# Performance work log

Hardware: AMD Instinct MI355X
Metric: run time of the kernel (lower is better)

## Reference

```python
import jax, jax.numpy as jnp
import numpy as np


def setup_inputs() -> dict:
    key = jax.random.key(0)
    k1, k2, k3, k4, k5 = jax.random.split(key, 5)
    B, N, M, D = 4096, 2048, 2048, 9
    return {
        "x": jax.random.normal(k1, (B, N), dtype=jnp.float32),
        "eternal_weights": jax.random.normal(k2, (D, N, M), dtype=jnp.float32),
        "eternal_biases": jax.random.normal(k3, (M,), dtype=jnp.float32),
        "classical_weights": jax.random.normal(k4, (N, M), dtype=jnp.float32),
        "classical_biases": jax.random.normal(k5, (M,), dtype=jnp.float32),
    }


def _eternal_probs(eternal_weights, n, m):
    # The gate matrix is cos*I - sin*P + sin*P^T with P the circular shift,
    # so (gate @ s)[i] = cos*s[i] - sin*s[(i+1)%n] + sin*s[(i-1)%n].
    # Vectorize over all m output units at once: state is [m, n].
    state0 = jnp.full((m, n), 1.0 / np.sqrt(n), dtype=eternal_weights.dtype)
    angles = eternal_weights[:, :m, :3]  # [D, m, 3] -- weights[depth, j, 0/1/2]

    def gate(state, angle):  # angle: [m]
        c = jnp.cos(angle)[:, None]
        s = jnp.sin(angle)[:, None]
        return c * state - s * jnp.roll(state, -1, axis=1) + s * jnp.roll(state, 1, axis=1)

    def step(state, ang):  # ang: [m, 3] -- consciousness, intelligence, wisdom
        state = gate(state, ang[:, 0])
        state = gate(state, ang[:, 1])
        state = gate(state, ang[:, 2])
        return state, None

    state, _ = jax.lax.scan(step, state0, angles)
    return jnp.abs(state[:, 0]) ** 2  # [m]


def reference(x, eternal_weights, eternal_biases, classical_weights, classical_biases):
    # eternal_biases exists as a parameter in the original module but is unused in forward.
    n = x.shape[1]
    m = classical_weights.shape[1]
    classical = x @ classical_weights + classical_biases  # [B, m]
    probs = _eternal_probs(eternal_weights, n, m)  # [m], identical for every batch row
    return jnp.tanh(classical + probs[None, :])
```

## Files before the change

kernel.cpp:

```cpp
#include <hip/hip_runtime.h>
#include <hip/hip_fp8.h>
#include <stdint.h>

static constexpr int MM = 4096;
static constexpr int KK = 2048;
static constexpr int NN = 2048;

typedef float floatx16 __attribute__((ext_vector_type(16)));
typedef _Float16 f16x8 __attribute__((ext_vector_type(8)));
typedef unsigned short u16x8 __attribute__((ext_vector_type(8)));
typedef int intx4 __attribute__((ext_vector_type(4)));
typedef int intx8 __attribute__((ext_vector_type(8)));

__device__ __forceinline__ unsigned char f32_to_e4m3(float x) {
  __hip_fp8_e4m3 q(x);
  return (unsigned char)q.__x;
}
__device__ __forceinline__ float fast_tanh(float x) {
  float e = __expf(2.0f * x);
  return 1.0f - 2.0f / (e + 1.0f);
}
__device__ __forceinline__ unsigned short f32_to_f16_bits(float x) {
  union { _Float16 h; unsigned short u; } c; c.h = (_Float16)x;
  return c.u;
}
__device__ __forceinline__ float f16_bits_to_f32(unsigned short u) {
  union { _Float16 h; unsigned short u; } c; c.u = u;
  return (float)c.h;
}


__global__ __launch_bounds__(256) void prepass_kernel(
    const float* __restrict__ x, const float* __restrict__ E,
    const float* __restrict__ W, const float* __restrict__ cb,
    unsigned short* __restrict__ ahi, unsigned char* __restrict__ al8,
    unsigned short* __restrict__ bhi, unsigned char* __restrict__ bl8,
    float* __restrict__ bias2) {
  __shared__ float tile[64][65];
  const int blk = blockIdx.x;
  const int tid = threadIdx.x;

  if (blk < 2048) {
    int idx = blk * 256 + tid;
    int row = idx >> 7;
    int u = idx & 127;
    int g = u >> 2;
    int q = u & 3;
    const float4* s = (const float4*)(x + (size_t)row * KK + u * 16);
    float v[16];
#pragma unroll
    for (int p = 0; p < 4; p++) {
      float4 t = s[p];
      v[p * 4 + 0] = t.x; v[p * 4 + 1] = t.y; v[p * 4 + 2] = t.z; v[p * 4 + 3] = t.w;
    }
    unsigned short h[16];
    union { unsigned char b[16]; unsigned long long d[2]; } loq;
#pragma unroll
    for (int e = 0; e < 16; e++) {
      h[e] = f32_to_f16_bits(v[e]);
      float lo = v[e] - f16_bits_to_f32(h[e]);
      loq.b[e] = f32_to_e4m3(lo * 2048.0f);
    }
    size_t rb = (size_t)row * KK;
#pragma unroll
    for (int cc = 0; cc < 2; cc++) {
      int c8 = q * 2 + cc;
      int phys8 = (c8 + row + (row >> 3)) & 7;
      u16x8 o;
#pragma unroll
      for (int e = 0; e < 8; e++) o[e] = h[cc * 8 + e];
      *(u16x8*)(ahi + rb + g * 64 + phys8 * 8) = o;
    }
    {
      int sw = (row & 3) + ((row >> 2) & 3);
      int cA = (q >> 1) * 2;
      char* lb = (char*)al8 + rb + g * 64;
      *(unsigned long long*)(lb + (((cA + 0) + sw) & 3) * 16 + (q & 1) * 8) = loq.d[0];
      *(unsigned long long*)(lb + (((cA + 1) + sw) & 3) * 16 + (q & 1) * 8) = loq.d[1];
    }
  } else if (blk < 3072) {
    const int wb = blk - 2048;
    const int n0 = (wb & 31) * 64;
    const int k0 = (wb >> 5) * 64;
#pragma unroll
    for (int i = 0; i < 4; i++) {
      int t = tid + i * 256;
      int kr = t >> 4;
      int nc = (t & 15) * 4;
      const float4 vv = *(const float4*)(W + (size_t)(k0 + kr) * NN + n0 + nc);
      tile[nc + 0][kr] = vv.x;
      tile[nc + 1][kr] = vv.y;
      tile[nc + 2][kr] = vv.z;
      tile[nc + 3][kr] = vv.w;
    }
    __syncthreads();
    const int nl = tid >> 2;
    const int q = tid & 3;
    const int n = n0 + nl;
    float v[16];
    unsigned short h[16];
    union { unsigned char b[16]; unsigned long long d[2]; } loq;
#pragma unroll
    for (int e = 0; e < 16; e++) {
      v[e] = tile[nl][q * 16 + e];
      h[e] = f32_to_f16_bits(v[e]);
      float lo = v[e] - f16_bits_to_f32(h[e]);
      loq.b[e] = f32_to_e4m3(lo * 2048.0f);
    }
    size_t rb = (size_t)n * KK + k0;
#pragma unroll
    for (int cc = 0; cc < 2; cc++) {
      int c8 = q * 2 + cc;
      int phys8 = (c8 + n + (n >> 3)) & 7;
      u16x8 o;
#pragma unroll
      for (int e = 0; e < 8; e++) o[e] = h[cc * 8 + e];
      *(u16x8*)(bhi + rb + phys8 * 8) = o;
    }
    {
      int sw = (n & 3) + ((n >> 2) & 3);
      int cA = (q >> 1) * 2;
      char* lb = (char*)bl8 + rb;
      *(unsigned long long*)(lb + (((cA + 0) + sw) & 3) * 16 + (q & 1) * 8) = loq.d[0];
      *(unsigned long long*)(lb + (((cA + 1) + sw) & 3) * 16 + (q & 1) * 8) = loq.d[1];
    }
  } else {
    int i = (blk - 3072) * 256 + tid;
    if (i < NN) {
      float p = 1.0f / 2048.0f;
#pragma unroll
      for (int d = 0; d < 9; d++) {
        const float4 a = *(const float4*)(E + (size_t)d * (2048 * 2048) + (size_t)i * 2048);
        float c0 = cosf(a.x), c1 = cosf(a.y), c2 = cosf(a.z);
        p *= (c0 * c0) * (c1 * c1) * (c2 * c2);
      }
      bias2[i] = cb[i] + p;
    }
  }
}

#define GLL(dst, src)                                                        \
  __builtin_amdgcn_global_load_lds(                                          \
      (const __attribute__((address_space(1))) void*)(src),                  \
      (__attribute__((address_space(3))) void*)(dst), 16, 0, 0)

#define RD(S, CUR)                                                             \
  _Pragma("unroll") for (int t = 0; t < 2; t++) {                              \
    fa[S][t] = *(const f16x8*)(sAhB + (CUR) * 16384 + aho[S][t]);              \
    fb[S][t] = *(const f16x8*)(sBhB + (CUR) * 32768 + bho[S][t]);              \
  }

#define PERM(S)                                                                \
  _Pragma("unroll") for (int t = 0; t < 2; t++) {                              \
    const uint4 ua = *(const uint4*)&fa[S][t];                                 \
    fa8[t][2 * (S)]     = (int)__builtin_amdgcn_perm(ua.y, ua.x, 0x07050301u); \
    fa8[t][2 * (S) + 1] = (int)__builtin_amdgcn_perm(ua.w, ua.z, 0x07050301u); \
    const uint4 ub = *(const uint4*)&fb[S][t];                                 \
    fb8[t][2 * (S)]     = (int)__builtin_amdgcn_perm(ub.y, ub.x, 0x07050301u); \
    fb8[t][2 * (S) + 1] = (int)__builtin_amdgcn_perm(ub.w, ub.z, 0x07050301u); \
  }

#define MFMA4(S)                                                               \
  __builtin_amdgcn_s_setprio(1);                                               \
  _Pragma("unroll") for (int i = 0; i < 2; i++)                                \
    _Pragma("unroll") for (int j = 0; j < 2; j++)                              \
      acc[i][j] = __builtin_amdgcn_mfma_f32_32x32x16_f16(fa[S][i], fb[S][j],   \
                                                         acc[i][j], 0, 0, 0); \
  __builtin_amdgcn_s_setprio(0);

#define BODY(CUR, NXT, KLO, KNX)                                               \
  {                                                                            \
    __builtin_amdgcn_s_barrier();    \
    __builtin_amdgcn_sched_barrier(0);                                         \
      \
      \
    intx4 la[2][2], lb[2][2];                                                  \
    _Pragma("unroll") for (int t = 0; t < 2; t++)                              \
      _Pragma("unroll") for (int c = 0; c < 2; c++) {                          \
        la[t][c] = *(const intx4*)(aloP[t][c] + (KLO));                        \
        lb[t][c] = *(const intx4*)(bloP[t][c] + (KLO));                        \
      }                                                                        \
    __builtin_amdgcn_sched_barrier(0);                                         \
                                    \
    _Pragma("unroll") for (int p = 0; p < 2; p++)                              \
      GLL(&sAh[NXT][p * 4096 + lds16], Ahi + a16 + (size_t)(KNX) + (size_t)(64 * p) * KK); \
    _Pragma("unroll") for (int p = 0; p < 4; p++)                              \
      GLL(&sBh[NXT][p * 4096 + lds16], Bhi + b16 + (size_t)(KNX) + (size_t)(64 * p) * KK); \
    asm volatile("s_waitcnt vmcnt(14)" ::: "memory");        \
    __builtin_amdgcn_sched_barrier(0);                                         \
    __builtin_amdgcn_s_barrier();           \
    __builtin_amdgcn_sched_barrier(0);                                         \
          \
    f16x8 fa[4][2], fb[4][2];                                                  \
    intx8 fa8[2], fb8[2];                                                      \
    RD(0, CUR) RD(1, CUR)                                                      \
    RD(2, CUR) PERM(0) MFMA4(0)                                                \
    RD(3, CUR) PERM(1) MFMA4(1)                                                \
    PERM(2) MFMA4(2)                                                           \
    PERM(3) MFMA4(3)                                                           \
    intx8 fal[2], fbl[2];                                                      \
    _Pragma("unroll") for (int t = 0; t < 2; t++) {                            \
      ((intx4*)&fal[t])[0] = la[t][0];                                         \
      ((intx4*)&fal[t])[1] = la[t][1];                                         \
      ((intx4*)&fbl[t])[0] = lb[t][0];                                         \
      ((intx4*)&fbl[t])[1] = lb[t][1];                                         \
    }                                                                          \
    __builtin_amdgcn_s_setprio(1);                                             \
    _Pragma("unroll") for (int i = 0; i < 2; i++)                              \
      _Pragma("unroll") for (int j = 0; j < 2; j++)                            \
        acc[i][j] = __builtin_amdgcn_mfma_scale_f32_32x32x64_f8f6f4(           \
            fal[i], fb8[j], acc[i][j], 0, 1, 0, 0x74747474, 0, 0x7f7f7f7f);    \
    _Pragma("unroll") for (int i = 0; i < 2; i++)                              \
      _Pragma("unroll") for (int j = 0; j < 2; j++)                            \
        acc[i][j] = __builtin_amdgcn_mfma_scale_f32_32x32x64_f8f6f4(           \
            fa8[i], fbl[j], acc[i][j], 1, 0, 0, 0x7f7f7f7f, 0, 0x74747474);    \
    __builtin_amdgcn_s_setprio(0);                                             \
  }

__global__ __launch_bounds__(512, 2) void gemm_tanh_kernel(
    const unsigned short* __restrict__ Ahi, const unsigned char* __restrict__ Al8,
    const unsigned short* __restrict__ Bhi, const unsigned char* __restrict__ Bl8,
    const float* __restrict__ bias2, float* __restrict__ out) {
  __shared__ __align__(16) unsigned short sAh[2][8192];
  __shared__ __align__(16) unsigned short sBh[2][16384];

  const int tid = threadIdx.x;
  const int lane = tid & 63;
  const int wave = tid >> 6;
  const int wm = (wave >> 2) * 64;
  const int wn = (wave & 3) * 64;

  const int id = blockIdx.x;
  const int bm = (id >> 3) * 128;
  const int bn = (id & 7) * 256;

  const size_t a16 = (size_t)(bm + (tid >> 3)) * KK + (tid & 7) * 8;
  const size_t b16 = (size_t)(bn + (tid >> 3)) * KK + (tid & 7) * 8;
  const int lds16 = tid * 8;

  const int r31 = lane & 31;
  const int half = lane >> 5;

  const char* sAhB = (const char*)(&sAh[0][0]);
  const char* sBhB = (const char*)(&sBh[0][0]);
  int aho[4][2], bho[4][2];
#pragma unroll
  for (int s = 0; s < 4; s++)
#pragma unroll
    for (int t = 0; t < 2; t++) {
      const int rowA = wm + t * 32 + r31;
      aho[s][t] = rowA * 128 + ((2 * s + half + rowA + (rowA >> 3)) & 7) * 16;
      const int rowB = wn + t * 32 + r31;
      bho[s][t] = rowB * 128 + ((2 * s + half + rowB + (rowB >> 3)) & 7) * 16;
    }
  const char* aloP[2][2];
  const char* bloP[2][2];
#pragma unroll
  for (int t = 0; t < 2; t++) {
    const int rowA = wm + t * 32 + r31;
    const int swA = (rowA & 3) + ((rowA >> 2) & 3);
    aloP[t][0] = (const char*)Al8 + (size_t)(bm + rowA) * KK + ((half + swA) & 3) * 16;
    aloP[t][1] = (const char*)Al8 + (size_t)(bm + rowA) * KK + ((2 + half + swA) & 3) * 16;
    const int rowB = wn + t * 32 + r31;
    const int swB = (rowB & 3) + ((rowB >> 2) & 3);
    bloP[t][0] = (const char*)Bl8 + (size_t)(bn + rowB) * KK + ((half + swB) & 3) * 16;
    bloP[t][1] = (const char*)Bl8 + (size_t)(bn + rowB) * KK + ((2 + half + swB) & 3) * 16;
  }

  floatx16 acc[2][2];
#pragma unroll
  for (int i = 0; i < 2; i++)
#pragma unroll
    for (int j = 0; j < 2; j++)
#pragma unroll
      for (int r = 0; r < 16; r++) acc[i][j][r] = 0.f;

#pragma unroll
  for (int p = 0; p < 2; p++)
    GLL(&sAh[0][p * 4096 + lds16], Ahi + a16 + (size_t)(64 * p) * KK);
#pragma unroll
  for (int p = 0; p < 4; p++)
    GLL(&sBh[0][p * 4096 + lds16], Bhi + b16 + (size_t)(64 * p) * KK);

  for (int kt = 0; kt < 32; kt += 2) {
    const int k0 = kt * 64;
    BODY(0, 1, k0, k0 + 64)
    BODY(1, 0, k0 + 64, (kt < 30) ? (k0 + 128) : 0)
  }
  asm volatile("s_waitcnt vmcnt(0)" ::: "memory");

#pragma unroll
  for (int j = 0; j < 2; j++) {
    int col = bn + wn + j * 32 + r31;
    float b2 = bias2[col];
#pragma unroll
    for (int i = 0; i < 2; i++) {
      int row0 = bm + wm + i * 32 + 4 * half;
#pragma unroll
      for (int r = 0; r < 16; r++) {
        int row = row0 + (r & 3) + 8 * (r >> 2);
        float val = acc[i][j][r] + b2;
        __builtin_nontemporal_store(fast_tanh(val), &out[(size_t)row * NN + col]);
      }
    }
  }
}

__global__ __launch_bounds__(256) void fallback_gemm(
    const float* __restrict__ x, const float* __restrict__ E,
    const float* __restrict__ W, const float* __restrict__ cb,
    float* __restrict__ out) {
  __shared__ float sA[16][16];
  __shared__ float sB[16][17];
  __shared__ float sbias[16];
  const int tx = threadIdx.x, ty = threadIdx.y;
  const int row = blockIdx.y * 16 + ty;
  const int col = blockIdx.x * 16 + tx;
  if (ty == 0) {
    float p = 1.0f / 2048.0f;
    for (int d = 0; d < 9; d++) {
      const float* a = E + (size_t)d * (2048 * 2048) + (size_t)col * 2048;
      for (int t = 0; t < 3; t++) { float c = cosf(a[t]); p *= c * c; }
    }
    sbias[tx] = p + cb[col];
  }
  float acc = 0.f;
  for (int k0 = 0; k0 < KK; k0 += 16) {
    __syncthreads();
    sA[ty][tx] = x[(size_t)row * KK + k0 + tx];
    sB[ty][tx] = W[(size_t)(k0 + ty) * NN + col];
    __syncthreads();
#pragma unroll
    for (int kk = 0; kk < 16; kk++) acc += sA[ty][kk] * sB[kk][tx];
  }
  out[(size_t)row * NN + col] = tanhf(acc + sbias[tx]);
}

extern "C" void kernel_launch(void* const* d_in, const int* in_sizes, int n_in,
                              void* d_out, int out_size, void* d_ws, size_t ws_size,
                              hipStream_t stream) {
  const float* x  = (const float*)d_in[0];
  const float* E  = (const float*)d_in[1];
  const float* W  = (const float*)d_in[3];
  const float* cb = (const float*)d_in[4];
  float* out = (float*)d_out;

  const size_t MB = 1024 * 1024;
  const size_t need = 36 * MB + NN * sizeof(float);
  if (ws_size < need) {
    fallback_gemm<<<dim3(NN / 16, MM / 16), dim3(16, 16), 0, stream>>>(x, E, W, cb, out);
    return;
  }

  char* ws = (char*)d_ws;
  unsigned short* Ahi = (unsigned short*)(ws);
  unsigned short* Bhi = (unsigned short*)(ws + 16 * MB);
  unsigned char* Al8  = (unsigned char*)(ws + 24 * MB);
  unsigned char* Bl8  = (unsigned char*)(ws + 32 * MB);
  float* bias2 = (float*)(ws + 36 * MB);

  prepass_kernel<<<dim3(3080), dim3(256), 0, stream>>>(
      x, E, W, cb, Ahi, Al8, Bhi, Bl8, bias2);
  gemm_tanh_kernel<<<dim3(256), dim3(512), 0, stream>>>(
      Ahi, Al8, Bhi, Bl8, bias2, out);
}
```

Before: 312.2 us.

## Shrink GEMM block tile to 128x128 with 4 waves and grouped block order

The block tile goes from 128x256 with 8 waves to 128x128 with 4 waves, doubling the grid to 512 blocks and halving the B shared buffer. Blocks are remapped into 4x4 groups to improve L2 reuse. All fp16 LDS reads and MFMAs are now issued before the byte permutes, instead of interleaving them. The aim is better occupancy and load balance across CUs, at the cost of less data reuse per block and more global traffic.

Result: faster. 297.4 us (-4.7%).

```diff
diff --git a/kernel.cpp b/kernel.cpp
--- a/kernel.cpp
+++ b/kernel.cpp
@@ -144,10 +144,12 @@
       (const __attribute__((address_space(1))) void*)(src),                  \
       (__attribute__((address_space(3))) void*)(dst), 16, 0, 0)
 
-#define RD(S, CUR)                                                             \
-  _Pragma("unroll") for (int t = 0; t < 2; t++) {                              \
-    fa[S][t] = *(const f16x8*)(sAhB + (CUR) * 16384 + aho[S][t]);              \
-    fb[S][t] = *(const f16x8*)(sBhB + (CUR) * 32768 + bho[S][t]);              \
+#define GLD(p) (*(const __attribute__((address_space(1))) intx4*)(p))
+
+#define RD(S, CUR)                                                            \
+  _Pragma("unroll") for (int t = 0; t < 2; t++) {                             \
+    fa[S][t] = *(const f16x8*)(sAhB + (CUR) * 16384 + aho[S][t]);             \
+    fb[S][t] = *(const f16x8*)(sBhB + (CUR) * 16384 + bho[S][t]);             \
   }
 
 #define PERM(S)                                                                \
@@ -159,14 +161,6 @@
     fb8[t][2 * (S)]     = (int)__builtin_amdgcn_perm(ub.y, ub.x, 0x07050301u); \
     fb8[t][2 * (S) + 1] = (int)__builtin_amdgcn_perm(ub.w, ub.z, 0x07050301u); \
   }
-
-#define MFMA4(S)                                                               \
-  __builtin_amdgcn_s_setprio(1);                                               \
-  _Pragma("unroll") for (int i = 0; i < 2; i++)                                \
-    _Pragma("unroll") for (int j = 0; j < 2; j++)                              \
-      acc[i][j] = __builtin_amdgcn_mfma_f32_32x32x16_f16(fa[S][i], fb[S][j],   \
-                                                         acc[i][j], 0, 0, 0); \
-  __builtin_amdgcn_s_setprio(0);
 
 #define BODY(CUR, NXT, KLO, KNX)                                               \
   {                                                                            \
@@ -177,27 +171,30 @@
     intx4 la[2][2], lb[2][2];                                                  \
     _Pragma("unroll") for (int t = 0; t < 2; t++)                              \
       _Pragma("unroll") for (int c = 0; c < 2; c++) {                          \
-        la[t][c] = *(const intx4*)(aloP[t][c] + (KLO));                        \
-        lb[t][c] = *(const intx4*)(bloP[t][c] + (KLO));                        \
+        la[t][c] = GLD(aloP[t][c] + (KLO));                                    \
+        lb[t][c] = GLD(bloP[t][c] + (KLO));                                    \
       }                                                                        \
     __builtin_amdgcn_sched_barrier(0);                                         \
                                     \
-    _Pragma("unroll") for (int p = 0; p < 2; p++)                              \
-      GLL(&sAh[NXT][p * 4096 + lds16], Ahi + a16 + (size_t)(KNX) + (size_t)(64 * p) * KK); \
-    _Pragma("unroll") for (int p = 0; p < 4; p++)                              \
-      GLL(&sBh[NXT][p * 4096 + lds16], Bhi + b16 + (size_t)(KNX) + (size_t)(64 * p) * KK); \
-    asm volatile("s_waitcnt vmcnt(14)" ::: "memory");        \
+    _Pragma("unroll") for (int p = 0; p < 4; p++) {                            \
+      GLL(&sAh[NXT][p * 2048 + lds16], Ahi + a16 + (size_t)(KNX) + (size_t)(32 * p) * KK); \
+      GLL(&sBh[NXT][p * 2048 + lds16], Bhi + b16 + (size_t)(KNX) + (size_t)(32 * p) * KK); \
+    }                                                                          \
+    asm volatile("s_waitcnt vmcnt(16)" ::: "memory");        \
     __builtin_amdgcn_sched_barrier(0);                                         \
     __builtin_amdgcn_s_barrier();           \
     __builtin_amdgcn_sched_barrier(0);                                         \
-          \
+        \
     f16x8 fa[4][2], fb[4][2];                                                  \
+    RD(0, CUR) RD(1, CUR) RD(2, CUR) RD(3, CUR)                                \
+    __builtin_amdgcn_s_setprio(1);                                             \
+    _Pragma("unroll") for (int s = 0; s < 4; s++)                              \
+      _Pragma("unroll") for (int i = 0; i < 2; i++)                            \
+        _Pragma("unroll") for (int j = 0; j < 2; j++)                          \
+          acc[i][j] = __builtin_amdgcn_mfma_f32_32x32x16_f16(fa[s][i], fb[s][j], acc[i][j], 0, 0, 0); \
+    __builtin_amdgcn_s_setprio(0);                                             \
     intx8 fa8[2], fb8[2];                                                      \
-    RD(0, CUR) RD(1, CUR)                                                      \
-    RD(2, CUR) PERM(0) MFMA4(0)                                                \
-    RD(3, CUR) PERM(1) MFMA4(1)                                                \
-    PERM(2) MFMA4(2)                                                           \
-    PERM(3) MFMA4(3)                                                           \
+    PERM(0) PERM(1) PERM(2) PERM(3)                                            \
     intx8 fal[2], fbl[2];                                                      \
     _Pragma("unroll") for (int t = 0; t < 2; t++) {                            \
       ((intx4*)&fal[t])[0] = la[t][0];                                         \
@@ -217,22 +214,23 @@
     __builtin_amdgcn_s_setprio(0);                                             \
   }
 
-__global__ __launch_bounds__(512, 2) void gemm_tanh_kernel(
+__global__ __launch_bounds__(256, 2) void gemm_tanh_kernel(
     const unsigned short* __restrict__ Ahi, const unsigned char* __restrict__ Al8,
     const unsigned short* __restrict__ Bhi, const unsigned char* __restrict__ Bl8,
     const float* __restrict__ bias2, float* __restrict__ out) {
   __shared__ __align__(16) unsigned short sAh[2][8192];
-  __shared__ __align__(16) unsigned short sBh[2][16384];
+  __shared__ __align__(16) unsigned short sBh[2][8192];
 
   const int tid = threadIdx.x;
   const int lane = tid & 63;
   const int wave = tid >> 6;
-  const int wm = (wave >> 2) * 64;
-  const int wn = (wave & 3) * 64;
+  const int wm = (wave >> 1) * 64;
+  const int wn = (wave & 1) * 64;
 
   const int id = blockIdx.x;
-  const int bm = (id >> 3) * 128;
-  const int bn = (id & 7) * 256;
+  const int cid = id >> 4, lid = id & 15;
+  const int bm = ((cid >> 2) * 4 + (lid >> 2)) * 128;
+  const int bn = ((cid & 3) * 4 + (lid & 3)) * 128;
 
   const size_t a16 = (size_t)(bm + (tid >> 3)) * KK + (tid & 7) * 8;
   const size_t b16 = (size_t)(bn + (tid >> 3)) * KK + (tid & 7) * 8;
@@ -276,11 +274,10 @@
       for (int r = 0; r < 16; r++) acc[i][j][r] = 0.f;
 
 #pragma unroll
-  for (int p = 0; p < 2; p++)
-    GLL(&sAh[0][p * 4096 + lds16], Ahi + a16 + (size_t)(64 * p) * KK);
-#pragma unroll
-  for (int p = 0; p < 4; p++)
-    GLL(&sBh[0][p * 4096 + lds16], Bhi + b16 + (size_t)(64 * p) * KK);
+  for (int p = 0; p < 4; p++) {
+    GLL(&sAh[0][p * 2048 + lds16], Ahi + a16 + (size_t)(32 * p) * KK);
+    GLL(&sBh[0][p * 2048 + lds16], Bhi + b16 + (size_t)(32 * p) * KK);
+  }
 
   for (int kt = 0; kt < 32; kt += 2) {
     const int k0 = kt * 64;
@@ -361,6 +358,6 @@
 
   prepass_kernel<<<dim3(3080), dim3(256), 0, stream>>>(
       x, E, W, cb, Ahi, Al8, Bhi, Bl8, bias2);
-  gemm_tanh_kernel<<<dim3(256), dim3(512), 0, stream>>>(
+  gemm_tanh_kernel<<<dim3(512), dim3(256), 0, stream>>>(
       Ahi, Al8, Bhi, Bl8, bias2, out);
 }
```
